# Kernel tuning notes

Hardware: AMD Instinct MI355X
Metric: run time of the kernel (lower is better)

The kernel has to match this reference:

```python
import jax, jax.numpy as jnp
import numpy as np

HEAD_DIM = 128
N_HEADS = 32
N_KV_HEADS = 8
ROPE_BASE = 500000.0
QK_EPS = 1e-6


def _rope_cos_sin(position_ids, head_dim, base, dtype):
    # position_ids: [B, S] int -> cos/sin [B, 1, S, head_dim]
    inv_freq = 1.0 / (base ** (jnp.arange(0, head_dim, 2, dtype=jnp.float32) / head_dim))
    freqs = position_ids.astype(jnp.float32)[..., None] * inv_freq  # [B, S, D/2]
    emb = jnp.concatenate([freqs, freqs], axis=-1)  # [B, S, D]
    return jnp.cos(emb).astype(dtype)[:, None], jnp.sin(emb).astype(dtype)[:, None]


def _rotate_half(x):
    x1, x2 = jnp.split(x, 2, axis=-1)
    return jnp.concatenate([-x2, x1], axis=-1)


def _qk_norm(x, scale, eps):
    # L2 norm (not RMS): scale * x / (||x||_2 + eps)
    norm = jnp.sqrt(jnp.sum(x * x, axis=-1, keepdims=True))
    return scale * x / (norm + eps)


def setup_inputs() -> dict:
    key = jax.random.key(0)
    ks = jax.random.split(key, 7)
    B, S, H = 1, 2048, 4096
    kv_dim = N_KV_HEADS * HEAD_DIM
    return {
        "hidden_states": jax.random.normal(ks[0], (B, S, H), dtype=jnp.float32),
        "position_ids": jnp.broadcast_to(jnp.arange(S, dtype=jnp.int64 if jax.config.jax_enable_x64 else jnp.int32), (B, S)),
        "Wq": jax.random.normal(ks[1], (H, H), dtype=jnp.float32) * (H ** -0.5),
        "Wk": jax.random.normal(ks[2], (kv_dim, H), dtype=jnp.float32) * (H ** -0.5),
        "Wv": jax.random.normal(ks[3], (kv_dim, H), dtype=jnp.float32) * (H ** -0.5),
        "Wo": jax.random.normal(ks[4], (H, H), dtype=jnp.float32) * (H ** -0.5),
        "q_scale": jnp.ones((HEAD_DIM,), dtype=jnp.float32),
        "k_scale": jnp.ones((HEAD_DIM,), dtype=jnp.float32),
    }


def reference(hidden_states, position_ids, Wq, Wk, Wv, Wo, q_scale, k_scale):
    B, S, H = hidden_states.shape
    scaling = 1.0 / np.sqrt(HEAD_DIM)

    # projections (torch Linear: y = x @ W.T)
    q = (hidden_states @ Wq.T).reshape(B, S, N_HEADS, HEAD_DIM).transpose(0, 2, 1, 3)
    k = (hidden_states @ Wk.T).reshape(B, S, N_KV_HEADS, HEAD_DIM).transpose(0, 2, 1, 3)
    v = (hidden_states @ Wv.T).reshape(B, S, N_KV_HEADS, HEAD_DIM).transpose(0, 2, 1, 3)

    cos, sin = _rope_cos_sin(position_ids, HEAD_DIM, ROPE_BASE, q.dtype)
    q = q * cos + _rotate_half(q) * sin
    k = k * cos + _rotate_half(k) * sin

    q = _qk_norm(q, q_scale, QK_EPS)
    k = _qk_norm(k, k_scale, QK_EPS)

    # GQA: repeat kv heads to match query heads
    n_rep = N_HEADS // N_KV_HEADS
    k = jnp.repeat(k, n_rep, axis=1)  # [B, n_heads, S, D]
    v = jnp.repeat(v, n_rep, axis=1)

    # causal SDPA
    scores = jnp.einsum("bhqd,bhkd->bhqk", q, k) * scaling
    causal = jnp.tril(jnp.ones((S, S), dtype=bool))
    scores = jnp.where(causal, scores, jnp.finfo(scores.dtype).min)
    attn = jax.nn.softmax(scores, axis=-1)
    out = jnp.einsum("bhqk,bhkd->bhqd", attn, v)  # [B, H, S, D]

    out = out.transpose(0, 2, 1, 3).reshape(B, S, H)
    return out @ Wo.T
```

## Files before the change

### kernel.cpp

```cpp
#include <hip/hip_runtime.h>
#include <math.h>

typedef unsigned short u16;
typedef unsigned int u32;
typedef __attribute__((ext_vector_type(8))) short bf16x8;
typedef __attribute__((ext_vector_type(4))) float f32x4;

#define S_LEN 2048
#define HID 4096
#define NH 32
#define NKV 8
#define HD 128
#define QS 6144

__device__ __forceinline__ u16 f2bf(float f) {
  u32 u = __float_as_uint(f);
  u32 r = (u + 0x7FFFu + ((u >> 16) & 1u)) >> 16;
  return (u16)r;
}
__device__ __forceinline__ float bf2f(u16 v) {
  return __uint_as_float(((u32)v) << 16);
}
__device__ __forceinline__ f32x4 mfma16(bf16x8 a, bf16x8 b, f32x4 c) {
  return __builtin_amdgcn_mfma_f32_16x16x32_bf16(a, b, c, 0, 0, 0);
}
__device__ __forceinline__ void async16(const u16* g, u16* l) {
  __builtin_amdgcn_global_load_lds(
      (__attribute__((address_space(1))) void*)g,
      (__attribute__((address_space(3))) void*)l, 16, 0, 0);
}
#if __has_builtin(__builtin_amdgcn_exp2f)
#define EXP2(x) __builtin_amdgcn_exp2f(x)
#else
#define EXP2(x) exp2f(x)
#endif

#define VMC(n) asm volatile("s_waitcnt vmcnt(" #n ")" ::: "memory")
#define BAR __builtin_amdgcn_s_barrier()
#define CFENCE asm volatile("" ::: "memory")

__global__ __launch_bounds__(256) void conv_hs(const float* __restrict__ hs,
                                               u16* __restrict__ dst) {
  int i = blockIdx.x * 256 + threadIdx.x;
  float4 v = ((const float4*)hs)[i];
  ushort4 o;
  o.x = f2bf(v.x); o.y = f2bf(v.y); o.z = f2bf(v.z); o.w = f2bf(v.w);
  ((ushort4*)dst)[i] = o;
}


#define DSA(dst, qi, d)                                                    \
  {                                                                        \
    const u16* p_ = As + (d)*16384 + (wm * 64 + (qi)*32 + cl) * 64;        \
    _Pragma("unroll") for (int ii = 0; ii < 2; ii++)                       \
        _Pragma("unroll") for (int kk = 0; kk < 2; kk++)                   \
            dst[ii][kk] =                                                  \
        *(const bf16x8*)(p_ + ii * 1024 + ((c0 ^ (kk << 2)) << 3));        \
  }

#define DSB(dst, qj, d)                                                    \
  {                                                                        \
    const u16* p_ =                                                        \
        Bs + (d)*BSTR + (wn * (BN / 2) + (qj) * (BN / 4) + cl) * 64;       \
    _Pragma("unroll") for (int jj = 0; jj < NJ; jj++)                      \
        _Pragma("unroll") for (int kk = 0; kk < 2; kk++)                   \
            dst[jj][kk] =                                                  \
        *(const bf16x8*)(p_ + jj * 1024 + ((c0 ^ (kk << 2)) << 3));        \
  }

#define MM(qi, qj, asrc, bsrc)                                             \
  {                                                                        \
    _Pragma("unroll") for (int kk = 0; kk < 2; kk++)                       \
        _Pragma("unroll") for (int ii = 0; ii < 2; ii++)                   \
            _Pragma("unroll") for (int jj = 0; jj < NJ; jj++)              \
                acc[(qi)*2 + ii][(qj)*NJ + jj] =                           \
        mfma16(asrc[ii][kk], bsrc[jj][kk], acc[(qi)*2 + ii][(qj)*NJ + jj]);\
  }

#define PH2(MMA1, MMA2)                                          \
  {                                                              \
    BAR;                                                         \
    MMA1; MMA2;                                                  \
    BAR;                                                         \
  }

#define VMCP2()                             \
  do {                                      \
    if constexpr (NJ == 3) VMC(10);         \
    else VMC(8);                            \
  } while (0)

template <int NJ>
__global__ __launch_bounds__(512, 2) void gemm4p(
    const u16* __restrict__ A, const float* __restrict__ W0,
    const float* __restrict__ W1, const float* __restrict__ W2,
    int nb1, int nb2, u16* __restrict__ Cb, float* __restrict__ Cf,
    int N, int K) {
  constexpr int BN = NJ * 64;
  constexpr int BSTR = BN * 64;
  extern __shared__ u16 lds[];
  u16* As = lds;
  u16* Bs = lds + 32768;
  const int tid = threadIdx.x;
  const int lane = tid & 63, wv = tid >> 6;
  const int cl = lane & 15, qd = lane >> 4;
  const int wm = wv >> 1, wn = wv & 1;
  const int c0 = qd ^ (cl & 7);

  const int cpx = gridDim.x >> 3;
  const int swz = (blockIdx.x & 7) * cpx + (blockIdx.x >> 3);
  const int m0 = (swz & 7) * 256;
  const int n0 = (swz >> 3) * BN;

  u32 aof[4];
#pragma unroll
  for (int q = 0; q < 4; q++) {
    int r = q * 64 + wv * 8 + (lane >> 3);
    int c = (lane & 7) ^ (r & 7);
    aof[q] = (u32)(m0 + r) * K + c * 8;
  }
  const int sbo = wv * 512;

  const float* bptr[2 * NJ];
  u32 bwr[2 * NJ];
#pragma unroll
  for (int rq = 0; rq < 2 * NJ; rq++) {
    int rl = rq * 32 + (tid >> 4);
    int gc = tid & 15;
    int row = n0 + rl;
    const float* p = (row < nb1) ? (W0 + (size_t)row * K)
                   : (row < nb2) ? (W1 + (size_t)(row - nb1) * K)
                                 : (W2 + (size_t)(row - nb2) * K);
    bptr[rq] = p + gc * 4;
    bwr[rq] = (u32)rl * 64 + (((gc >> 1) ^ (rl & 7)) * 8) + ((gc & 1) * 4);
  }

  auto STAll = [&](int tt, int d) {
#pragma unroll
    for (int q = 0; q < 4; q++)
      async16(A + (size_t)tt * 64 + aof[q], As + d * 16384 + q * 4096 + sbo);
  };

  float4 bv[2 * NJ];
  auto ldB = [&]() {
#pragma unroll
    for (int rq = 0; rq < 2 * NJ; rq++) {
      bv[rq] = *(const float4*)bptr[rq];
      bptr[rq] += 64;
    }
  };
  auto wrB = [&](int d) {
#pragma unroll
    for (int rq = 0; rq < 2 * NJ; rq++) {
      u32 lo = (u32)f2bf(bv[rq].x) | ((u32)f2bf(bv[rq].y) << 16);
      u32 hi = (u32)f2bf(bv[rq].z) | ((u32)f2bf(bv[rq].w) << 16);
      uint2 wd;
      wd.x = lo;
      wd.y = hi;
      *(uint2*)(Bs + d * BSTR + bwr[rq]) = wd;
    }
    CFENCE;
  };

  f32x4 acc[4][2 * NJ];
  f32x4 zz = {0.f, 0.f, 0.f, 0.f};
#pragma unroll
  for (int i = 0; i < 4; i++)
#pragma unroll
    for (int j = 0; j < 2 * NJ; j++) acc[i][j] = zz;
  bf16x8 A0r[2][2], A1r[2][2], B0r[NJ][2], B1r[NJ][2];

  const int NT = K >> 6;

  STAll(0, 0);
  STAll(1, 1);
  ldB();
  wrB(0);
  VMC(4);
  asm volatile("s_waitcnt lgkmcnt(0)" ::: "memory");
  BAR;

  for (int it = 0; it < (NT >> 1); ++it) {
    const int t = it * 2;
    const bool s2 = (t + 2) < NT;
    ldB();
    DSA(A0r, 0, 0); DSA(A1r, 1, 0); DSB(B0r, 0, 0);
    wrB(1);
    PH2(MM(0, 0, A0r, B0r), MM(1, 0, A1r, B0r));
    DSB(B1r, 1, 0);
    if (s2) {
      ldB();
      STAll(t + 2, 0);
      VMCP2();
    } else {
      VMC(0);
    }
    PH2(MM(0, 1, A0r, B1r), MM(1, 1, A1r, B1r));
    DSA(A0r, 0, 1); DSA(A1r, 1, 1); DSB(B0r, 0, 1);
    if (s2) wrB(0);
    PH2(MM(0, 0, A0r, B0r), MM(1, 0, A1r, B0r));
    DSB(B1r, 1, 1);
    if (s2) {
      STAll(t + 3, 1);
      VMC(4);
    } else {
      VMC(0);
    }
    PH2(MM(0, 1, A0r, B1r), MM(1, 1, A1r, B1r));
  }

#pragma unroll
  for (int i = 0; i < 4; i++)
#pragma unroll
    for (int j = 0; j < 2 * NJ; j++) {
      int row = m0 + wm * 64 + i * 16 + qd * 4;
      int col = n0 + wn * (BN / 2) + (j / NJ) * (BN / 4) + (j % NJ) * 16 + cl;
#pragma unroll
      for (int r = 0; r < 4; r++) {
        float v = acc[i][j][r];
        if (Cb) Cb[(size_t)(row + r) * N + col] = f2bf(v);
        else    Cf[(size_t)(row + r) * N + col] = v;
      }
    }
}

__global__ __launch_bounds__(256) void rope_l2norm(
    u16* __restrict__ x, const int* __restrict__ pos_ids,
    const float* __restrict__ scale, int hmask, int hshift, int stride) {
  const int lane = threadIdx.x & 63;
  const int wv = threadIdx.x >> 6;
  const int idx = blockIdx.x * 4 + wv;
  const int s = idx >> hshift;
  const int h = idx & hmask;
  u16* p = x + (size_t)s * stride + h * HD;
  const float pos = (float)pos_ids[s];
  const float inv = expf((float)lane * -0.20503692777194264f);
  float sn, cs;
  sincosf(pos * inv, &sn, &cs);
  float a = bf2f(p[lane]);
  float b = bf2f(p[lane + 64]);
  float ra = a * cs - b * sn;
  float rb = b * cs + a * sn;
  float ss = ra * ra + rb * rb;
#pragma unroll
  for (int off = 32; off >= 1; off >>= 1) ss += __shfl_xor(ss, off, 64);
  float rd = 1.0f / (sqrtf(ss) + 1e-6f);
  p[lane] = f2bf(scale[lane] * ra * rd);
  p[lane + 64] = f2bf(scale[lane + 64] * rb * rd);
}

__global__ __launch_bounds__(256) void transpose_v(const u16* __restrict__ v,
                                                   u16* __restrict__ vt) {
  __shared__ u16 t[64][65];
  const int r = threadIdx.x >> 6;
  const int c = threadIdx.x & 63;
  const int s0 = blockIdx.x * 64, d0 = blockIdx.y * 64;
#pragma unroll
  for (int i = 0; i < 16; i++) {
    int row = i * 4 + r;
    t[row][c] = v[(size_t)(s0 + row) * QS + d0 + c];
  }
  __syncthreads();
#pragma unroll
  for (int i = 0; i < 16; i++) {
    int row = i * 4 + r;
    vt[(size_t)(d0 + row) * S_LEN + s0 + c] = t[c][row];
  }
}

#define PLD 68

__global__ __launch_bounds__(512) void flash_attn(
    const u16* __restrict__ QKV, const u16* __restrict__ Vt,
    u16* __restrict__ O) {
  extern __shared__ u16 alds[];
  u16* Ks = alds;
  u16* Vs = alds + 16384;
  u16* Ps = alds + 32768;
  const int tid = threadIdx.x;
  const int lane = tid & 63, wv = tid >> 6;
  const int cl = lane & 15, qd = lane >> 4;
  const int h = blockIdx.y;
  const int kvh = h >> 2;
  const float es = 0.12751629240081506f;

  const u16* Kbase = QKV + 4096 + kvh * HD;
  const u16* Vbase = Vt + (size_t)kvh * HD * S_LEN;

  auto stage = [&](int kt, int d) {
#pragma unroll
    for (int q = 0; q < 2; q++) {
      int c = q * 512 + wv * 64 + lane;
      int kr = c >> 4, kg = (c & 15) ^ (kr & 15);
      async16(Kbase + (size_t)(kt * 64 + kr) * QS + kg * 8,
              Ks + d * 8192 + (q * 512 + wv * 64) * 8);
      int vr = c >> 3, vg = (c & 7) ^ (vr & 7);
      async16(Vbase + (size_t)vr * S_LEN + kt * 64 + vg * 8,
              Vs + d * 8192 + (q * 512 + wv * 64) * 8);
    }
  };

  for (int half = 0; half < 2; half++) {
    const int qbi = half ? (15 - (int)blockIdx.x) : (int)blockIdx.x;
    const int q0 = qbi * 128;

    bf16x8 aQ[4];
    {
      const u16* qrow =
          QKV + (size_t)(q0 + wv * 16 + cl) * QS + h * HD + qd * 8;
#pragma unroll
      for (int kk = 0; kk < 4; kk++) aQ[kk] = *(const bf16x8*)(qrow + kk * 32);
    }

    f32x4 oacc[8];
    f32x4 zz = {0.f, 0.f, 0.f, 0.f};
#pragma unroll
    for (int n = 0; n < 8; n++) oacc[n] = zz;
    float lsum[4] = {0.f, 0.f, 0.f, 0.f};

    const int row_min = q0 + wv * 16;
    const int ktmax = 2 * qbi + 1;

    int cur = 0;
    stage(0, 0);
    for (int kt = 0; kt <= ktmax; kt++) {
      if (kt < ktmax) stage(kt + 1, cur ^ 1);
      if (kt == 0) {
        VMC(4);
        BAR;
      }
      const int koff = cur * 8192;

      if (kt * 64 <= row_min + 15) {
        f32x4 sacc[4];
#pragma unroll
        for (int j = 0; j < 4; j++) sacc[j] = zz;
#pragma unroll
        for (int kk = 0; kk < 4; kk++) {
#pragma unroll
          for (int j = 0; j < 4; j++) {
            int row = j * 16 + cl;
            int ch = (kk * 4 + qd) ^ (row & 15);
            bf16x8 bK = *(const bf16x8*)&Ks[koff + row * 128 + ch * 8];
            sacc[j] = mfma16(aQ[kk], bK, sacc[j]);
          }
        }

        float pm[4][4];
        if (kt * 64 + 63 > row_min) {
          const int grow = row_min + qd * 4;
#pragma unroll
          for (int j = 0; j < 4; j++) {
            int gcol = kt * 64 + j * 16 + cl;
#pragma unroll
            for (int r = 0; r < 4; r++)
              pm[j][r] = (gcol <= grow + r) ? EXP2(sacc[j][r] * es) : 0.f;
          }
        } else {
#pragma unroll
          for (int j = 0; j < 4; j++)
#pragma unroll
            for (int r = 0; r < 4; r++) pm[j][r] = EXP2(sacc[j][r] * es);
        }
#pragma unroll
        for (int j = 0; j < 4; j++)
#pragma unroll
          for (int r = 0; r < 4; r++) lsum[r] += pm[j][r];

#pragma unroll
        for (int j = 0; j < 4; j++)
#pragma unroll
          for (int r = 0; r < 4; r++)
            Ps[(wv * 16 + qd * 4 + r) * PLD + j * 16 + cl] = f2bf(pm[j][r]);
        __asm__ volatile("s_waitcnt lgkmcnt(0)" ::: "memory");

#pragma unroll
        for (int kk = 0; kk < 2; kk++) {
          bf16x8 aP =
              *(const bf16x8*)&Ps[(wv * 16 + cl) * PLD + kk * 32 + qd * 8];
#pragma unroll
          for (int n = 0; n < 8; n++) {
            int row = n * 16 + cl;
            int ch = (kk * 4 + qd) ^ (row & 7);
            bf16x8 bV = *(const bf16x8*)&Vs[koff + row * 64 + ch * 8];
            oacc[n] = mfma16(aP, bV, oacc[n]);
          }
        }
      }

      VMC(0);
      BAR;
      cur ^= 1;
    }

#pragma unroll
    for (int r = 0; r < 4; r++) {
#pragma unroll
      for (int off = 8; off >= 1; off >>= 1)
        lsum[r] += __shfl_xor(lsum[r], off, 64);
    }
#pragma unroll
    for (int r = 0; r < 4; r++) {
      float il = 1.0f / lsum[r];
      int row = row_min + qd * 4 + r;
#pragma unroll
      for (int n = 0; n < 8; n++)
        O[(size_t)row * HID + h * HD + n * 16 + cl] = f2bf(oacc[n][r] * il);
    }
  }
}

extern "C" void kernel_launch(void* const* d_in, const int* in_sizes, int n_in,
                              void* d_out, int out_size, void* d_ws, size_t ws_size,
                              hipStream_t stream) {
  const float* hs = (const float*)d_in[0];
  const int* pos = (const int*)d_in[1];
  const float* Wq = (const float*)d_in[2];
  const float* Wk = (const float*)d_in[3];
  const float* Wv = (const float*)d_in[4];
  const float* Wo = (const float*)d_in[5];
  const float* qsc = (const float*)d_in[6];
  const float* ksc = (const float*)d_in[7];
  float* out = (float*)d_out;
  char* ws = (char*)d_ws;
  const size_t MB = 1u << 20;

  u16* hs_b  = (u16*)(ws + 0 * MB);
  u16* qkv_b = (u16*)(ws + 64 * MB);
  u16* vt_b  = (u16*)(ws + 88 * MB);
  u16* o_b   = hs_b;

  static bool attr_set = false;
  if (!attr_set) {
    hipFuncSetAttribute(reinterpret_cast<const void*>(&gemm4p<3>),
                        hipFuncAttributeMaxDynamicSharedMemorySize, 114688);
    hipFuncSetAttribute(reinterpret_cast<const void*>(&gemm4p<2>),
                        hipFuncAttributeMaxDynamicSharedMemorySize, 98304);
    hipFuncSetAttribute(reinterpret_cast<const void*>(&flash_attn),
                        hipFuncAttributeMaxDynamicSharedMemorySize, 82944);
    attr_set = true;
  }

  conv_hs<<<8192, 256, 0, stream>>>(hs, hs_b);

  gemm4p<3><<<dim3(8 * (QS / 192)), 512, 114688, stream>>>(
      hs_b, Wq, Wk, Wv, 4096, 5120, qkv_b, nullptr, QS, HID);

  rope_l2norm<<<S_LEN * NH / 4, 256, 0, stream>>>(qkv_b, pos, qsc, NH - 1, 5, QS);
  rope_l2norm<<<S_LEN * NKV / 4, 256, 0, stream>>>(qkv_b + 4096, pos, ksc, NKV - 1, 3, QS);
  transpose_v<<<dim3(S_LEN / 64, (NKV * HD) / 64), 256, 0, stream>>>(qkv_b + 5120, vt_b);

  flash_attn<<<dim3(8, NH), 512, 82944, stream>>>(qkv_b, vt_b, o_b);

  gemm4p<2><<<dim3(8 * (HID / 128)), 512, 98304, stream>>>(
      o_b, Wo, Wo, Wo, HID, HID, nullptr, out, HID, HID);
}
```

Baseline: 523.6 us.

## Double-buffer fp32 weight register loads with separate even/odd staging

The GEMM's fp32 weight tiles now use two register staging sets (even and odd). Each set is loaded one half-step earlier and converted/written to LDS later, so global load latency is spread across more MFMA phases. The waitcnt values and explicit lgkmcnt waits are adjusted to match. This costs extra VGPRs for the second float4 array, which may pressure occupancy at launch bounds 512,2, and the changed vmcnt counts must still track the outstanding loads correctly.

```diff
diff --git a/kernel.cpp b/kernel.cpp
--- a/kernel.cpp
+++ b/kernel.cpp
@@ -36,8 +36,8 @@
 #endif
 
 #define VMC(n) asm volatile("s_waitcnt vmcnt(" #n ")" ::: "memory")
+#define LGKM0 asm volatile("s_waitcnt lgkmcnt(0)" ::: "memory")
 #define BAR __builtin_amdgcn_s_barrier()
-#define CFENCE asm volatile("" ::: "memory")
 
 __global__ __launch_bounds__(256) void conv_hs(const float* __restrict__ hs,
                                                u16* __restrict__ dst) {
@@ -83,12 +83,6 @@
     MMA1; MMA2;                                                  \
     BAR;                                                         \
   }
-
-#define VMCP2()                             \
-  do {                                      \
-    if constexpr (NJ == 3) VMC(10);         \
-    else VMC(8);                            \
-  } while (0)
 
 template <int NJ>
 __global__ __launch_bounds__(512, 2) void gemm4p(
@@ -141,25 +135,38 @@
       async16(A + (size_t)tt * 64 + aof[q], As + d * 16384 + q * 4096 + sbo);
   };
 
-  float4 bv[2 * NJ];
-  auto ldB = [&]() {
+  float4 bvE[2 * NJ], bvO[2 * NJ];
+  auto ldBE = [&]() {
 #pragma unroll
     for (int rq = 0; rq < 2 * NJ; rq++) {
-      bv[rq] = *(const float4*)bptr[rq];
+      bvE[rq] = *(const float4*)bptr[rq];
       bptr[rq] += 64;
     }
   };
-  auto wrB = [&](int d) {
+  auto ldBO = [&]() {
 #pragma unroll
     for (int rq = 0; rq < 2 * NJ; rq++) {
-      u32 lo = (u32)f2bf(bv[rq].x) | ((u32)f2bf(bv[rq].y) << 16);
-      u32 hi = (u32)f2bf(bv[rq].z) | ((u32)f2bf(bv[rq].w) << 16);
+      bvO[rq] = *(const float4*)bptr[rq];
+      bptr[rq] += 64;
+    }
+  };
+  auto wrBE = [&](int d) {
+#pragma unroll
+    for (int rq = 0; rq < 2 * NJ; rq++) {
       uint2 wd;
-      wd.x = lo;
-      wd.y = hi;
+      wd.x = (u32)f2bf(bvE[rq].x) | ((u32)f2bf(bvE[rq].y) << 16);
+      wd.y = (u32)f2bf(bvE[rq].z) | ((u32)f2bf(bvE[rq].w) << 16);
       *(uint2*)(Bs + d * BSTR + bwr[rq]) = wd;
     }
-    CFENCE;
+  };
+  auto wrBO = [&](int d) {
+#pragma unroll
+    for (int rq = 0; rq < 2 * NJ; rq++) {
+      uint2 wd;
+      wd.x = (u32)f2bf(bvO[rq].x) | ((u32)f2bf(bvO[rq].y) << 16);
+      wd.y = (u32)f2bf(bvO[rq].z) | ((u32)f2bf(bvO[rq].w) << 16);
+      *(uint2*)(Bs + d * BSTR + bwr[rq]) = wd;
+    }
   };
 
   f32x4 acc[4][2 * NJ];
@@ -172,40 +179,43 @@
 
   const int NT = K >> 6;
 
+  ldBE();
   STAll(0, 0);
   STAll(1, 1);
-  ldB();
-  wrB(0);
-  VMC(4);
-  asm volatile("s_waitcnt lgkmcnt(0)" ::: "memory");
+  wrBE(0);
+  ldBO();
+  VMC(10);
+  LGKM0;
   BAR;
 
   for (int it = 0; it < (NT >> 1); ++it) {
     const int t = it * 2;
     const bool s2 = (t + 2) < NT;
-    ldB();
+    wrBO(1);
     DSA(A0r, 0, 0); DSA(A1r, 1, 0); DSB(B0r, 0, 0);
-    wrB(1);
+    LGKM0;
     PH2(MM(0, 0, A0r, B0r), MM(1, 0, A1r, B0r));
     DSB(B1r, 1, 0);
     if (s2) {
-      ldB();
+      ldBE();
       STAll(t + 2, 0);
-      VMCP2();
+      VMC(10);
     } else {
       VMC(0);
     }
     PH2(MM(0, 1, A0r, B1r), MM(1, 1, A1r, B1r));
     DSA(A0r, 0, 1); DSA(A1r, 1, 1); DSB(B0r, 0, 1);
-    if (s2) wrB(0);
     PH2(MM(0, 0, A0r, B0r), MM(1, 0, A1r, B0r));
     DSB(B1r, 1, 1);
     if (s2) {
+      wrBE(0);
+      ldBO();
       STAll(t + 3, 1);
-      VMC(4);
+      VMC(10);
     } else {
       VMC(0);
     }
+    LGKM0;
     PH2(MM(0, 1, A0r, B1r), MM(1, 1, A1r, B1r));
   }
 
```

After: 758.9 us. 1.45x slower.
